# Kernel tuning notes

Measured on AMD Instinct MI355X. Metric: run time of the kernel, lower is better.

The kernel has to match this reference:

```python
import math
import jax, jax.numpy as jnp
import numpy as np

B, S, D, H = 4, 2048, 1024, 16
DK = D // H
THETA = 10000.0


def _rope(xh, pos):
    # xh: [B, H, S, DK], pos: [S]
    half = jnp.arange(0, DK, 2, dtype=jnp.float32) / DK
    inv_freq = THETA ** (-half)                      # [DK/2]
    ang = pos.astype(jnp.float32)[:, None] * inv_freq  # [S, DK/2]
    cos, sin = jnp.cos(ang).astype(xh.dtype), jnp.sin(ang).astype(xh.dtype)
    x1, x2 = xh[..., 0::2], xh[..., 1::2]
    r1 = x1 * cos - x2 * sin
    r2 = x1 * sin + x2 * cos
    return jnp.stack([r1, r2], axis=-1).reshape(xh.shape)


def setup_inputs() -> dict:
    key = jax.random.key(0)
    kx, kq, kk, kv, ko = jax.random.split(key, 5)
    std = 0.02
    x = jax.random.normal(kx, (B, S, D), jnp.float32)
    wq = jax.random.normal(kq, (D, D), jnp.float32) * std
    wk = jax.random.normal(kk, (D, D), jnp.float32) * std
    wv = jax.random.normal(kv, (D, D), jnp.float32) * std
    wo = jax.random.normal(ko, (D, D), jnp.float32) * std
    token_positions = jnp.arange(S, dtype=jnp.int32)
    return {"x": x, "wq": wq, "wk": wk, "wv": wv, "wo": wo,
            "token_positions": token_positions}


def reference(x, wq, wk, wv, wo, token_positions):
    # bias-free linear projections: y = x @ W^T (torch Linear convention)
    q = x @ wq.T
    k = x @ wk.T
    v = x @ wv.T
    # split heads: [B, S, D] -> [B, H, S, DK]
    to_heads = lambda t: t.reshape(B, S, H, DK).transpose(0, 2, 1, 3)
    qh, kh, vh = to_heads(q), to_heads(k), to_heads(v)
    qh = _rope(qh, token_positions)
    kh = _rope(kh, token_positions)
    scores = jnp.einsum('bhqd,bhkd->bhqk', qh, kh) / math.sqrt(DK)
    causal = jnp.tril(jnp.ones((S, S), dtype=bool))
    scores = jnp.where(causal, scores, -jnp.inf)
    attn = jax.nn.softmax(scores, axis=-1)
    out = jnp.einsum('bhqk,bhkd->bhqd', attn, vh)       # [B, H, S, DK]
    out = out.transpose(0, 2, 1, 3).reshape(B, S, D)    # merge heads
    return out @ wo.T
```

## Files before the change

kernel.cpp:

```cpp
#include <hip/hip_runtime.h>

#define B_ 4
#define S_ 2048
#define D_ 1024
#define H_ 16
#define DK_ 64
#define M_ (B_*S_)
#define K_ D_
#define N_ D_

typedef unsigned short u16;
typedef unsigned int u32;
typedef __bf16 bf16x8 __attribute__((ext_vector_type(8)));
typedef float f32x4 __attribute__((ext_vector_type(4)));
typedef u32 u32x4v __attribute__((ext_vector_type(4)));

#define EXP2F(x) __builtin_amdgcn_exp2f(x)

__device__ __forceinline__ u16 f2bf(float f) {
    u32 u = __builtin_bit_cast(u32, f);
    u += 0x7fff + ((u >> 16) & 1);
    return (u16)(u >> 16);
}
__device__ __forceinline__ float bf2f(u16 h) {
    u32 u = ((u32)h) << 16;
    return __builtin_bit_cast(float, u);
}
__device__ __forceinline__ u32 pack_trunc(float a, float b) {
    return (__builtin_bit_cast(u32, a) >> 16) | (__builtin_bit_cast(u32, b) & 0xffff0000u);
}

#define GLDS16(g, l) __builtin_amdgcn_global_load_lds( \
    (__attribute__((address_space(1))) void*)(g),      \
    (__attribute__((address_space(3))) void*)(l), 16, 0, 0)

__global__ __launch_bounds__(256) void cvt_x(const float* __restrict__ in,
                                             u16* __restrict__ out, int n4) {
    const int i = blockIdx.x * 256 + threadIdx.x;
    if (i >= n4) return;
    const float4 f = *(const float4*)(in + (size_t)i * 4);
    u32 p0 = (u32)f2bf(f.x) | ((u32)f2bf(f.y) << 16);
    u32 p1 = (u32)f2bf(f.z) | ((u32)f2bf(f.w) << 16);
    *(uint2*)(out + (size_t)i * 4) = make_uint2(p0, p1);
}

__global__ __launch_bounds__(256) void cvt_w4(
    const float* __restrict__ w0, const float* __restrict__ w1,
    const float* __restrict__ w2, const float* __restrict__ w3,
    u16* __restrict__ o0, u16* __restrict__ o1,
    u16* __restrict__ o2, u16* __restrict__ o3) {
    const int wi = blockIdx.y;
    const float* in = (wi == 0) ? w0 : (wi == 1) ? w1 : (wi == 2) ? w2 : w3;
    u16* out       = (wi == 0) ? o0 : (wi == 1) ? o1 : (wi == 2) ? o2 : o3;
    const int i = blockIdx.x * 256 + threadIdx.x;
    const float4 f = *(const float4*)(in + (size_t)i * 4);
    u32 p0 = (u32)f2bf(f.x) | ((u32)f2bf(f.y) << 16);
    u32 p1 = (u32)f2bf(f.z) | ((u32)f2bf(f.w) << 16);
    *(uint2*)(out + (size_t)i * 4) = make_uint2(p0, p1);
}

template <int MODE>
__device__ __forceinline__ void gemm_tile(const u16* __restrict__ A,
                                          const u16* __restrict__ Bm,
                                          void* __restrict__ Cv) {
    __shared__ u16 As[128 * 32];
    __shared__ u16 Bs[128 * 32];
    const int tid  = threadIdx.x;
    const int wave = tid >> 6, lane = tid & 63;
    const int m0 = blockIdx.y * 128, n0 = blockIdx.x * 128;
    const int wm = wave & 1, wn = wave >> 1;
    const int quad = lane >> 4, mcol = lane & 15;

    const int c0 = wave, c1 = wave + 4;
    const int r0 = c0 * 16 + (lane >> 2), r1 = c1 * 16 + (lane >> 2);
    const int kb = (lane & 3) * 8;
    const u16* ga0 = A  + (size_t)(m0 + r0) * K_ + kb;
    const u16* ga1 = A  + (size_t)(m0 + r1) * K_ + kb;
    const u16* gb0 = Bm + (size_t)(n0 + r0) * K_ + kb;
    const u16* gb1 = Bm + (size_t)(n0 + r1) * K_ + kb;
    u16* la0 = &As[c0 * 512];
    u16* la1 = &As[c1 * 512];
    u16* lb0 = &Bs[c0 * 512];
    u16* lb1 = &Bs[c1 * 512];

    f32x4 acc[4][4];
#pragma unroll
    for (int i = 0; i < 4; i++)
#pragma unroll
        for (int j = 0; j < 4; j++) acc[i][j] = f32x4{0.f, 0.f, 0.f, 0.f};

    for (int kt = 0; kt < K_; kt += 32) {
        __syncthreads();
        GLDS16(ga0, la0); GLDS16(ga1, la1);
        GLDS16(gb0, lb0); GLDS16(gb1, lb1);
        ga0 += 32; ga1 += 32; gb0 += 32; gb1 += 32;
        __syncthreads();

        bf16x8 af[4], bfr[4];
#pragma unroll
        for (int i = 0; i < 4; i++) {
            af[i]  = *(const bf16x8*)&As[(size_t)(wm * 64 + i * 16 + mcol) * 32 + quad * 8];
            bfr[i] = *(const bf16x8*)&Bs[(size_t)(wn * 64 + i * 16 + mcol) * 32 + quad * 8];
        }
#pragma unroll
        for (int i = 0; i < 4; i++)
#pragma unroll
            for (int j = 0; j < 4; j++)
                acc[i][j] = __builtin_amdgcn_mfma_f32_16x16x32_bf16(
                    af[i], bfr[j], acc[i][j], 0, 0, 0);
    }

#pragma unroll
    for (int i = 0; i < 4; i++) {
        const int row = m0 + wm * 64 + i * 16 + quad * 4;
#pragma unroll
        for (int j = 0; j < 4; j++) {
            const int col = n0 + wn * 64 + j * 16 + mcol;
            if constexpr (MODE == 2) {
                const int hh = col >> 6, dd = col & 63;
                const int bb = row >> 11, ss = row & 2047;
                const u32 lo = (u32)f2bf(acc[i][j][0]) | ((u32)f2bf(acc[i][j][1]) << 16);
                const u32 hi = (u32)f2bf(acc[i][j][2]) | ((u32)f2bf(acc[i][j][3]) << 16);
                *(uint2*)((u16*)Cv + ((size_t)((bb * H_ + hh) * DK_ + dd)) * S_ + ss) =
                    make_uint2(lo, hi);
            } else {
#pragma unroll
                for (int r = 0; r < 4; r++) {
                    if constexpr (MODE == 1)
                        ((float*)Cv)[(size_t)(row + r) * N_ + col] = acc[i][j][r];
                    else
                        ((u16*)Cv)[(size_t)(row + r) * N_ + col] = f2bf(acc[i][j][r]);
                }
            }
        }
    }
}

__global__ __launch_bounds__(256) void gemm_qk_kernel(
    const u16* __restrict__ x,
    const u16* __restrict__ wq, const u16* __restrict__ wk,
    u16* __restrict__ q, u16* __restrict__ k) {
    const u16* Bm = (blockIdx.z == 0) ? wq : wk;
    u16* C        = (blockIdx.z == 0) ? q  : k;
    gemm_tile<0>(x, Bm, C);
}

__global__ __launch_bounds__(256) void gemm_v_kernel(
    const u16* __restrict__ x, const u16* __restrict__ wv, u16* __restrict__ vt) {
    gemm_tile<2>(x, wv, vt);
}

__global__ __launch_bounds__(256) void gemm_out_kernel(
    const u16* __restrict__ o, const u16* __restrict__ wo, float* __restrict__ out) {
    gemm_tile<1>(o, wo, out);
}

__global__ __launch_bounds__(256) void rope_qk(u16* __restrict__ q,
                                               u16* __restrict__ k,
                                               const int* __restrict__ pos) {
    const int idx = blockIdx.x * 256 + threadIdx.x;
    const int i = idx & 31;
    const int h = (idx >> 5) & (H_ - 1);
    const int s = (idx >> 9) & (S_ - 1);
    const int b = idx >> 20;
    const float p = (float)pos[s];
    const float inv = exp2f((float)i * (-13.287712379549449f / 32.f));
    const float ang = p * inv;
    float sn, cs;
    __sincosf(ang, &sn, &cs);
    const float QSC = 0.18033688011112042f;
    const size_t off = ((size_t)(b * S_ + s)) * D_ + h * DK_ + 2 * i;
    {
        float x1 = bf2f(q[off]), x2 = bf2f(q[off + 1]);
        q[off]     = f2bf((x1 * cs - x2 * sn) * QSC);
        q[off + 1] = f2bf((x1 * sn + x2 * cs) * QSC);
    }
    {
        float x1 = bf2f(k[off]), x2 = bf2f(k[off + 1]);
        k[off]     = f2bf(x1 * cs - x2 * sn);
        k[off + 1] = f2bf(x1 * sn + x2 * cs);
    }
}

__global__ __launch_bounds__(256) void attn_kernel(
    const u16* __restrict__ q, const u16* __restrict__ k,
    const u16* __restrict__ vt, u16* __restrict__ o) {
    __shared__ u16 Ks[64][72];
    __shared__ u16 Vs[64][72];

    const int tid = threadIdx.x, wave = tid >> 6, lane = tid & 63;
    const int flat = blockIdx.x;
    const int qt = flat >> 6;
    const int h = flat & (H_ - 1);
    const int b = (flat >> 4) & 3;
    const int q0 = qt * 128;
    const int quad = lane >> 4, mcol = lane & 15;
    const int wq0 = q0 + wave * 32;

    bf16x8 qf[2][2];
#pragma unroll
    for (int g = 0; g < 2; g++) {
        const u16* qs = q + ((size_t)(b * S_ + wq0 + g * 16 + mcol)) * D_ + h * DK_ + quad * 8;
        qf[g][0] = *(const bf16x8*)qs;
        qf[g][1] = *(const bf16x8*)(qs + 32);
    }

    float m[2] = {-1e30f, -1e30f}, l[2] = {0.f, 0.f};
    f32x4 oacc[2][4];
#pragma unroll
    for (int g = 0; g < 2; g++)
#pragma unroll
        for (int dn = 0; dn < 4; dn++) oacc[g][dn] = f32x4{0.f, 0.f, 0.f, 0.f};

    const int rr2 = tid >> 2, ch2 = (tid & 3) * 16;
    const int prr = (rr2 & 35) | ((rr2 & 12) << 1) | ((rr2 & 16) >> 2);
    const u16* krow = k + ((size_t)(b * S_ + prr)) * D_ + h * DK_ + ch2;
    const u16* vrow = vt + ((size_t)((b * H_ + h) * DK_ + rr2)) * S_ + ch2;
    const int jmax = 2 * qt + 1;

    uint4 kr0 = *(const uint4*)(krow);
    uint4 kr1 = *(const uint4*)(krow + 8);
    uint4 vr0 = *(const uint4*)(vrow);
    uint4 vr1 = *(const uint4*)(vrow + 8);

    for (int j = 0; j <= jmax; j++) {
        __syncthreads();
        *(uint4*)&Ks[rr2][ch2]     = kr0;
        *(uint4*)&Ks[rr2][ch2 + 8] = kr1;
        *(uint4*)&Vs[rr2][ch2]     = vr0;
        *(uint4*)&Vs[rr2][ch2 + 8] = vr1;
        __syncthreads();

        if (j < jmax) {
            kr0 = *(const uint4*)(krow + (size_t)(j + 1) * 64 * D_);
            kr1 = *(const uint4*)(krow + (size_t)(j + 1) * 64 * D_ + 8);
            vr0 = *(const uint4*)(vrow + (j + 1) * 64);
            vr1 = *(const uint4*)(vrow + (j + 1) * 64 + 8);
        }

        if (j * 64 > wq0 + 31) continue;

        f32x4 st[2][4];
#pragma unroll
        for (int n = 0; n < 4; n++) {
            bf16x8 kf0 = *(const bf16x8*)&Ks[n * 16 + mcol][quad * 8];
            bf16x8 kf1 = *(const bf16x8*)&Ks[n * 16 + mcol][32 + quad * 8];
            f32x4 z0 = f32x4{0.f, 0.f, 0.f, 0.f};
            z0 = __builtin_amdgcn_mfma_f32_16x16x32_bf16(kf0, qf[0][0], z0, 0, 0, 0);
            z0 = __builtin_amdgcn_mfma_f32_16x16x32_bf16(kf1, qf[0][1], z0, 0, 0, 0);
            st[0][n] = z0;
            f32x4 z1 = f32x4{0.f, 0.f, 0.f, 0.f};
            z1 = __builtin_amdgcn_mfma_f32_16x16x32_bf16(kf0, qf[1][0], z1, 0, 0, 0);
            z1 = __builtin_amdgcn_mfma_f32_16x16x32_bf16(kf1, qf[1][1], z1, 0, 0, 0);
            st[1][n] = z1;
        }

        if (j * 64 + 63 > wq0) {
#pragma unroll
            for (int g = 0; g < 2; g++) {
                const int qg = wq0 + g * 16 + mcol;
#pragma unroll
                for (int n = 0; n < 4; n++) {
                    const int tb = j * 64 + ((n >> 1) << 5) + ((n & 1) << 2) + quad * 8;
#pragma unroll
                    for (int r = 0; r < 4; r++)
                        if (tb + r > qg) st[g][n][r] = -1e30f;
                }
            }
        }

#pragma unroll
        for (int g = 0; g < 2; g++) {
            float mx = st[g][0][0];
#pragma unroll
            for (int n = 0; n < 4; n++)
#pragma unroll
                for (int r = 0; r < 4; r++) mx = fmaxf(mx, st[g][n][r]);
            mx = fmaxf(mx, __shfl_xor(mx, 16));
            mx = fmaxf(mx, __shfl_xor(mx, 32));
            float al = 1.f;
            const bool need = !__all(mx <= m[g] + 8.f);
            if (need) {
                const float mnew = fmaxf(m[g], mx);
                al = EXP2F(m[g] - mnew);
                m[g] = mnew;
            }
            float sum = 0.f;
#pragma unroll
            for (int n = 0; n < 4; n++)
#pragma unroll
                for (int r = 0; r < 4; r++) {
                    const float p = EXP2F(st[g][n][r] - m[g]);
                    st[g][n][r] = p;
                    sum += p;
                }
            sum += __shfl_xor(sum, 16);
            sum += __shfl_xor(sum, 32);
            l[g] = l[g] * al + sum;
            if (need) {
                float alphaT[4];
#pragma unroll
                for (int r = 0; r < 4; r++) alphaT[r] = __shfl(al, quad * 4 + r);
#pragma unroll
                for (int dn = 0; dn < 4; dn++)
#pragma unroll
                    for (int r = 0; r < 4; r++) oacc[g][dn][r] *= alphaT[r];
            }
        }

        bf16x8 pf[2][2];
#pragma unroll
        for (int g = 0; g < 2; g++) {
            u32x4v w0, w1;
            w0[0] = pack_trunc(st[g][0][0], st[g][0][1]);
            w0[1] = pack_trunc(st[g][0][2], st[g][0][3]);
            w0[2] = pack_trunc(st[g][1][0], st[g][1][1]);
            w0[3] = pack_trunc(st[g][1][2], st[g][1][3]);
            w1[0] = pack_trunc(st[g][2][0], st[g][2][1]);
            w1[1] = pack_trunc(st[g][2][2], st[g][2][3]);
            w1[2] = pack_trunc(st[g][3][0], st[g][3][1]);
            w1[3] = pack_trunc(st[g][3][2], st[g][3][3]);
            pf[g][0] = __builtin_bit_cast(bf16x8, w0);
            pf[g][1] = __builtin_bit_cast(bf16x8, w1);
        }

#pragma unroll
        for (int dn = 0; dn < 4; dn++) {
            bf16x8 vf0 = *(const bf16x8*)&Vs[dn * 16 + mcol][quad * 8];
            bf16x8 vf1 = *(const bf16x8*)&Vs[dn * 16 + mcol][32 + quad * 8];
#pragma unroll
            for (int g = 0; g < 2; g++) {
                oacc[g][dn] = __builtin_amdgcn_mfma_f32_16x16x32_bf16(pf[g][0], vf0, oacc[g][dn], 0, 0, 0);
                oacc[g][dn] = __builtin_amdgcn_mfma_f32_16x16x32_bf16(pf[g][1], vf1, oacc[g][dn], 0, 0, 0);
            }
        }
    }

#pragma unroll
    for (int g = 0; g < 2; g++) {
        float linv[4];
#pragma unroll
        for (int r = 0; r < 4; r++) linv[r] = 1.f / __shfl(l[g], quad * 4 + r);
#pragma unroll
        for (int dn = 0; dn < 4; dn++)
#pragma unroll
            for (int r = 0; r < 4; r++) {
                const int row = wq0 + g * 16 + quad * 4 + r;
                o[((size_t)(b * S_ + row)) * D_ + h * DK_ + dn * 16 + mcol] =
                    f2bf(oacc[g][dn][r] * linv[r]);
            }
    }
}

extern "C" void kernel_launch(void* const* d_in, const int* in_sizes, int n_in,
                              void* d_out, int out_size, void* d_ws, size_t ws_size,
                              hipStream_t stream) {
    const float* x  = (const float*)d_in[0];
    const float* wq = (const float*)d_in[1];
    const float* wk = (const float*)d_in[2];
    const float* wv = (const float*)d_in[3];
    const float* wo = (const float*)d_in[4];
    const int*   tp = (const int*)d_in[5];
    float* out = (float*)d_out;

    u16* ws = (u16*)d_ws;
    const size_t NE = (size_t)M_ * D_;
    const size_t WE = (size_t)N_ * K_;
    u16* xb  = ws;
    u16* wqb = ws + NE;
    u16* wkb = wqb + WE;
    u16* wvb = wkb + WE;
    u16* wob = wvb + WE;
    u16* qb  = wob + WE;
    u16* kb  = qb + NE;
    u16* vtb = (u16*)d_out;
    u16* ob  = xb;

    dim3 blk(256);
    cvt_x<<<dim3((int)(NE / 1024)), blk, 0, stream>>>(x, xb, (int)(NE / 4));
    cvt_w4<<<dim3((int)(WE / 1024), 4), blk, 0, stream>>>(wq, wk, wv, wo, wqb, wkb, wvb, wob);

    gemm_qk_kernel<<<dim3(N_ / 128, M_ / 128, 2), blk, 0, stream>>>(xb, wqb, wkb, qb, kb);
    gemm_v_kernel<<<dim3(N_ / 128, M_ / 128, 1), blk, 0, stream>>>(xb, wvb, vtb);
    rope_qk<<<dim3((B_ * S_ * H_ * 32) / 256), blk, 0, stream>>>(qb, kb, tp);
    attn_kernel<<<dim3((S_ / 128) * H_ * B_), blk, 0, stream>>>(qb, kb, vtb, ob);
    gemm_out_kernel<<<dim3(N_ / 128, M_ / 128, 1), blk, 0, stream>>>(ob, wob, out);
}
```

Measured before the change: 305.6 us.

## Pair causal query tiles per block, XOR-swizzle LDS, raise MFMA priority

Each attention block now handles two query tiles, qp and 15-qp, one after the other, so every block does the same amount of causal work. This halves the grid to 512 blocks. K/V shared memory drops the padded 72-column rows in favour of an unpadded 64-column layout with an XOR swizzle on 16-byte chunks, which avoids bank conflicts and uses less LDS. s_setprio raises wave priority around the MFMA sections. The cost is fewer blocks, and so less parallelism across the CUs, plus a serial second pass in each block.

```diff
diff --git a/kernel.cpp b/kernel.cpp
--- a/kernel.cpp
+++ b/kernel.cpp
@@ -185,170 +185,185 @@
 __global__ __launch_bounds__(256) void attn_kernel(
     const u16* __restrict__ q, const u16* __restrict__ k,
     const u16* __restrict__ vt, u16* __restrict__ o) {
-    __shared__ u16 Ks[64][72];
-    __shared__ u16 Vs[64][72];
+    __shared__ u16 Ks[64 * 64];
+    __shared__ u16 Vs[64 * 64];
 
     const int tid = threadIdx.x, wave = tid >> 6, lane = tid & 63;
     const int flat = blockIdx.x;
-    const int qt = flat >> 6;
+    const int qp = flat >> 6;
     const int h = flat & (H_ - 1);
     const int b = (flat >> 4) & 3;
-    const int q0 = qt * 128;
     const int quad = lane >> 4, mcol = lane & 15;
-    const int wq0 = q0 + wave * 32;
-
-    bf16x8 qf[2][2];
-#pragma unroll
-    for (int g = 0; g < 2; g++) {
-        const u16* qs = q + ((size_t)(b * S_ + wq0 + g * 16 + mcol)) * D_ + h * DK_ + quad * 8;
-        qf[g][0] = *(const bf16x8*)qs;
-        qf[g][1] = *(const bf16x8*)(qs + 32);
-    }
-
-    float m[2] = {-1e30f, -1e30f}, l[2] = {0.f, 0.f};
-    f32x4 oacc[2][4];
-#pragma unroll
-    for (int g = 0; g < 2; g++)
-#pragma unroll
-        for (int dn = 0; dn < 4; dn++) oacc[g][dn] = f32x4{0.f, 0.f, 0.f, 0.f};
-
-    const int rr2 = tid >> 2, ch2 = (tid & 3) * 16;
+    const int srd = mcol & 7;
+
+    const int rr2 = tid >> 2, cc2 = tid & 3;
+    const int sw = rr2 & 7;
+    const int so0 = rr2 * 64 + (((cc2 * 2)     ^ sw) << 3);
+    const int so1 = rr2 * 64 + (((cc2 * 2 + 1) ^ sw) << 3);
     const int prr = (rr2 & 35) | ((rr2 & 12) << 1) | ((rr2 & 16) >> 2);
+    const int ch2 = cc2 * 16;
     const u16* krow = k + ((size_t)(b * S_ + prr)) * D_ + h * DK_ + ch2;
     const u16* vrow = vt + ((size_t)((b * H_ + h) * DK_ + rr2)) * S_ + ch2;
-    const int jmax = 2 * qt + 1;
-
-    uint4 kr0 = *(const uint4*)(krow);
-    uint4 kr1 = *(const uint4*)(krow + 8);
-    uint4 vr0 = *(const uint4*)(vrow);
-    uint4 vr1 = *(const uint4*)(vrow + 8);
-
-    for (int j = 0; j <= jmax; j++) {
-        __syncthreads();
-        *(uint4*)&Ks[rr2][ch2]     = kr0;
-        *(uint4*)&Ks[rr2][ch2 + 8] = kr1;
-        *(uint4*)&Vs[rr2][ch2]     = vr0;
-        *(uint4*)&Vs[rr2][ch2 + 8] = vr1;
-        __syncthreads();
-
-        if (j < jmax) {
-            kr0 = *(const uint4*)(krow + (size_t)(j + 1) * 64 * D_);
-            kr1 = *(const uint4*)(krow + (size_t)(j + 1) * 64 * D_ + 8);
-            vr0 = *(const uint4*)(vrow + (j + 1) * 64);
-            vr1 = *(const uint4*)(vrow + (j + 1) * 64 + 8);
+
+    for (int pass = 0; pass < 2; pass++) {
+        const int qt = pass ? (15 - qp) : qp;
+        const int q0 = qt * 128;
+        const int wq0 = q0 + wave * 32;
+        const int jmax = 2 * qt + 1;
+
+        bf16x8 qf[2][2];
+#pragma unroll
+        for (int g = 0; g < 2; g++) {
+            const u16* qs = q + ((size_t)(b * S_ + wq0 + g * 16 + mcol)) * D_ + h * DK_ + quad * 8;
+            qf[g][0] = *(const bf16x8*)qs;
+            qf[g][1] = *(const bf16x8*)(qs + 32);
         }
 
-        if (j * 64 > wq0 + 31) continue;
-
-        f32x4 st[2][4];
-#pragma unroll
-        for (int n = 0; n < 4; n++) {
-            bf16x8 kf0 = *(const bf16x8*)&Ks[n * 16 + mcol][quad * 8];
-            bf16x8 kf1 = *(const bf16x8*)&Ks[n * 16 + mcol][32 + quad * 8];
-            f32x4 z0 = f32x4{0.f, 0.f, 0.f, 0.f};
-            z0 = __builtin_amdgcn_mfma_f32_16x16x32_bf16(kf0, qf[0][0], z0, 0, 0, 0);
-            z0 = __builtin_amdgcn_mfma_f32_16x16x32_bf16(kf1, qf[0][1], z0, 0, 0, 0);
-            st[0][n] = z0;
-            f32x4 z1 = f32x4{0.f, 0.f, 0.f, 0.f};
-            z1 = __builtin_amdgcn_mfma_f32_16x16x32_bf16(kf0, qf[1][0], z1, 0, 0, 0);
-            z1 = __builtin_amdgcn_mfma_f32_16x16x32_bf16(kf1, qf[1][1], z1, 0, 0, 0);
-            st[1][n] = z1;
+        float m[2] = {-1e30f, -1e30f}, l[2] = {0.f, 0.f};
+        f32x4 oacc[2][4];
+#pragma unroll
+        for (int g = 0; g < 2; g++)
+#pragma unroll
+            for (int dn = 0; dn < 4; dn++) oacc[g][dn] = f32x4{0.f, 0.f, 0.f, 0.f};
+
+        uint4 kr0 = *(const uint4*)(krow);
+        uint4 kr1 = *(const uint4*)(krow + 8);
+        uint4 vr0 = *(const uint4*)(vrow);
+        uint4 vr1 = *(const uint4*)(vrow + 8);
+
+        for (int j = 0; j <= jmax; j++) {
+            __syncthreads();
+            *(uint4*)&Ks[so0] = kr0;
+            *(uint4*)&Ks[so1] = kr1;
+            *(uint4*)&Vs[so0] = vr0;
+            *(uint4*)&Vs[so1] = vr1;
+            __syncthreads();
+
+            if (j < jmax) {
+                kr0 = *(const uint4*)(krow + (size_t)(j + 1) * 64 * D_);
+                kr1 = *(const uint4*)(krow + (size_t)(j + 1) * 64 * D_ + 8);
+                vr0 = *(const uint4*)(vrow + (j + 1) * 64);
+                vr1 = *(const uint4*)(vrow + (j + 1) * 64 + 8);
+            }
+
+            if (j * 64 > wq0 + 31) continue;
+
+            f32x4 st[2][4];
+            __builtin_amdgcn_s_setprio(1);
+#pragma unroll
+            for (int n = 0; n < 4; n++) {
+                const u16* kl = &Ks[(n * 16 + mcol) * 64];
+                bf16x8 kf0 = *(const bf16x8*)&kl[(quad ^ srd) << 3];
+                bf16x8 kf1 = *(const bf16x8*)&kl[((quad | 4) ^ srd) << 3];
+                f32x4 z0 = f32x4{0.f, 0.f, 0.f, 0.f};
+                z0 = __builtin_amdgcn_mfma_f32_16x16x32_bf16(kf0, qf[0][0], z0, 0, 0, 0);
+                z0 = __builtin_amdgcn_mfma_f32_16x16x32_bf16(kf1, qf[0][1], z0, 0, 0, 0);
+                st[0][n] = z0;
+                f32x4 z1 = f32x4{0.f, 0.f, 0.f, 0.f};
+                z1 = __builtin_amdgcn_mfma_f32_16x16x32_bf16(kf0, qf[1][0], z1, 0, 0, 0);
+                z1 = __builtin_amdgcn_mfma_f32_16x16x32_bf16(kf1, qf[1][1], z1, 0, 0, 0);
+                st[1][n] = z1;
+            }
+            __builtin_amdgcn_s_setprio(0);
+
+            if (j * 64 + 63 > wq0) {
+#pragma unroll
+                for (int g = 0; g < 2; g++) {
+                    const int qg = wq0 + g * 16 + mcol;
+#pragma unroll
+                    for (int n = 0; n < 4; n++) {
+                        const int tb = j * 64 + ((n >> 1) << 5) + ((n & 1) << 2) + quad * 8;
+#pragma unroll
+                        for (int r = 0; r < 4; r++)
+                            if (tb + r > qg) st[g][n][r] = -1e30f;
+                    }
+                }
+            }
+
+#pragma unroll
+            for (int g = 0; g < 2; g++) {
+                float mx = st[g][0][0];
+#pragma unroll
+                for (int n = 0; n < 4; n++)
+#pragma unroll
+                    for (int r = 0; r < 4; r++) mx = fmaxf(mx, st[g][n][r]);
+                mx = fmaxf(mx, __shfl_xor(mx, 16));
+                mx = fmaxf(mx, __shfl_xor(mx, 32));
+                float al = 1.f;
+                const bool need = !__all(mx <= m[g] + 8.f);
+                if (need) {
+                    const float mnew = fmaxf(m[g], mx);
+                    al = EXP2F(m[g] - mnew);
+                    m[g] = mnew;
+                }
+                float sum = 0.f;
+#pragma unroll
+                for (int n = 0; n < 4; n++)
+#pragma unroll
+                    for (int r = 0; r < 4; r++) {
+                        const float p = EXP2F(st[g][n][r] - m[g]);
+                        st[g][n][r] = p;
+                        sum += p;
+                    }
+                sum += __shfl_xor(sum, 16);
+                sum += __shfl_xor(sum, 32);
+                l[g] = l[g] * al + sum;
+                if (need) {
+                    float alphaT[4];
+#pragma unroll
+                    for (int r = 0; r < 4; r++) alphaT[r] = __shfl(al, quad * 4 + r);
+#pragma unroll
+                    for (int dn = 0; dn < 4; dn++)
+#pragma unroll
+                        for (int r = 0; r < 4; r++) oacc[g][dn][r] *= alphaT[r];
+                }
+            }
+
+            bf16x8 pf[2][2];
+#pragma unroll
+            for (int g = 0; g < 2; g++) {
+                u32x4v w0, w1;
+                w0[0] = pack_trunc(st[g][0][0], st[g][0][1]);
+                w0[1] = pack_trunc(st[g][0][2], st[g][0][3]);
+                w0[2] = pack_trunc(st[g][1][0], st[g][1][1]);
+                w0[3] = pack_trunc(st[g][1][2], st[g][1][3]);
+                w1[0] = pack_trunc(st[g][2][0], st[g][2][1]);
+                w1[1] = pack_trunc(st[g][2][2], st[g][2][3]);
+                w1[2] = pack_trunc(st[g][3][0], st[g][3][1]);
+                w1[3] = pack_trunc(st[g][3][2], st[g][3][3]);
+                pf[g][0] = __builtin_bit_cast(bf16x8, w0);
+                pf[g][1] = __builtin_bit_cast(bf16x8, w1);
+            }
+
+            __builtin_amdgcn_s_setprio(1);
+#pragma unroll
+            for (int dn = 0; dn < 4; dn++) {
+                const u16* vl = &Vs[(dn * 16 + mcol) * 64];
+                bf16x8 vf0 = *(const bf16x8*)&vl[(quad ^ srd) << 3];
+                bf16x8 vf1 = *(const bf16x8*)&vl[((quad | 4) ^ srd) << 3];
+#pragma unroll
+                for (int g = 0; g < 2; g++) {
+                    oacc[g][dn] = __builtin_amdgcn_mfma_f32_16x16x32_bf16(pf[g][0], vf0, oacc[g][dn], 0, 0, 0);
+                    oacc[g][dn] = __builtin_amdgcn_mfma_f32_16x16x32_bf16(pf[g][1], vf1, oacc[g][dn], 0, 0, 0);
+                }
+            }
+            __builtin_amdgcn_s_setprio(0);
         }
 
-        if (j * 64 + 63 > wq0) {
-#pragma unroll
-            for (int g = 0; g < 2; g++) {
-                const int qg = wq0 + g * 16 + mcol;
-#pragma unroll
-                for (int n = 0; n < 4; n++) {
-                    const int tb = j * 64 + ((n >> 1) << 5) + ((n & 1) << 2) + quad * 8;
-#pragma unroll
-                    for (int r = 0; r < 4; r++)
-                        if (tb + r > qg) st[g][n][r] = -1e30f;
-                }
-            }
+#pragma unroll
+        for (int g = 0; g < 2; g++) {
+            float linv[4];
+#pragma unroll
+            for (int r = 0; r < 4; r++) linv[r] = 1.f / __shfl(l[g], quad * 4 + r);
+#pragma unroll
+            for (int dn = 0; dn < 4; dn++)
+#pragma unroll
+                for (int r = 0; r < 4; r++) {
+                    const int row = wq0 + g * 16 + quad * 4 + r;
+                    o[((size_t)(b * S_ + row)) * D_ + h * DK_ + dn * 16 + mcol] =
+                        f2bf(oacc[g][dn][r] * linv[r]);
+                }
         }
-
-#pragma unroll
-        for (int g = 0; g < 2; g++) {
-            float mx = st[g][0][0];
-#pragma unroll
-            for (int n = 0; n < 4; n++)
-#pragma unroll
-                for (int r = 0; r < 4; r++) mx = fmaxf(mx, st[g][n][r]);
-            mx = fmaxf(mx, __shfl_xor(mx, 16));
-            mx = fmaxf(mx, __shfl_xor(mx, 32));
-            float al = 1.f;
-            const bool need = !__all(mx <= m[g] + 8.f);
-            if (need) {
-                const float mnew = fmaxf(m[g], mx);
-                al = EXP2F(m[g] - mnew);
-                m[g] = mnew;
-            }
-            float sum = 0.f;
-#pragma unroll
-            for (int n = 0; n < 4; n++)
-#pragma unroll
-                for (int r = 0; r < 4; r++) {
-                    const float p = EXP2F(st[g][n][r] - m[g]);
-                    st[g][n][r] = p;
-                    sum += p;
-                }
-            sum += __shfl_xor(sum, 16);
-            sum += __shfl_xor(sum, 32);
-            l[g] = l[g] * al + sum;
-            if (need) {
-                float alphaT[4];
-#pragma unroll
-                for (int r = 0; r < 4; r++) alphaT[r] = __shfl(al, quad * 4 + r);
-#pragma unroll
-                for (int dn = 0; dn < 4; dn++)
-#pragma unroll
-                    for (int r = 0; r < 4; r++) oacc[g][dn][r] *= alphaT[r];
-            }
-        }
-
-        bf16x8 pf[2][2];
-#pragma unroll
-        for (int g = 0; g < 2; g++) {
-            u32x4v w0, w1;
-            w0[0] = pack_trunc(st[g][0][0], st[g][0][1]);
-            w0[1] = pack_trunc(st[g][0][2], st[g][0][3]);
-            w0[2] = pack_trunc(st[g][1][0], st[g][1][1]);
-            w0[3] = pack_trunc(st[g][1][2], st[g][1][3]);
-            w1[0] = pack_trunc(st[g][2][0], st[g][2][1]);
-            w1[1] = pack_trunc(st[g][2][2], st[g][2][3]);
-            w1[2] = pack_trunc(st[g][3][0], st[g][3][1]);
-            w1[3] = pack_trunc(st[g][3][2], st[g][3][3]);
-            pf[g][0] = __builtin_bit_cast(bf16x8, w0);
-            pf[g][1] = __builtin_bit_cast(bf16x8, w1);
-        }
-
-#pragma unroll
-        for (int dn = 0; dn < 4; dn++) {
-            bf16x8 vf0 = *(const bf16x8*)&Vs[dn * 16 + mcol][quad * 8];
-            bf16x8 vf1 = *(const bf16x8*)&Vs[dn * 16 + mcol][32 + quad * 8];
-#pragma unroll
-            for (int g = 0; g < 2; g++) {
-                oacc[g][dn] = __builtin_amdgcn_mfma_f32_16x16x32_bf16(pf[g][0], vf0, oacc[g][dn], 0, 0, 0);
-                oacc[g][dn] = __builtin_amdgcn_mfma_f32_16x16x32_bf16(pf[g][1], vf1, oacc[g][dn], 0, 0, 0);
-            }
-        }
-    }
-
-#pragma unroll
-    for (int g = 0; g < 2; g++) {
-        float linv[4];
-#pragma unroll
-        for (int r = 0; r < 4; r++) linv[r] = 1.f / __shfl(l[g], quad * 4 + r);
-#pragma unroll
-        for (int dn = 0; dn < 4; dn++)
-#pragma unroll
-            for (int r = 0; r < 4; r++) {
-                const int row = wq0 + g * 16 + quad * 4 + r;
-                o[((size_t)(b * S_ + row)) * D_ + h * DK_ + dn * 16 + mcol] =
-                    f2bf(oacc[g][dn][r] * linv[r]);
-            }
     }
 }
 
@@ -383,6 +398,6 @@
     gemm_qk_kernel<<<dim3(N_ / 128, M_ / 128, 2), blk, 0, stream>>>(xb, wqb, wkb, qb, kb);
     gemm_v_kernel<<<dim3(N_ / 128, M_ / 128, 1), blk, 0, stream>>>(xb, wvb, vtb);
     rope_qk<<<dim3((B_ * S_ * H_ * 32) / 256), blk, 0, stream>>>(qb, kb, tp);
-    attn_kernel<<<dim3((S_ / 128) * H_ * B_), blk, 0, stream>>>(qb, kb, vtb, ob);
+    attn_kernel<<<dim3((S_ / 128 / 2) * H_ * B_), blk, 0, stream>>>(qb, kb, vtb, ob);
     gemm_out_kernel<<<dim3(N_ / 128, M_ / 128, 1), blk, 0, stream>>>(ob, wob, out);
 }
```

Result: faster. 287.0 us (-6.1%).
